# Kernel optimization log

Hardware: AMD Instinct MI355X
Metric: run time of the kernel (lower is better)

Reference implementation:

```python
import jax, jax.numpy as jnp
import numpy as np

DIM, N_HEADS, HEAD_DIM, BASE = 1024, 16, 64, 10000.0
B, S = 2, 2048


def setup_inputs() -> dict:
    key = jax.random.key(0)
    ks = jax.random.split(key, 8)
    theta = (BASE ** (-jnp.arange(0, HEAD_DIM, 2, dtype=jnp.float32) / HEAD_DIM))  # [head_dim//2]
    s = 0.02
    return {
        "x": jax.random.normal(ks[0], (B, S, DIM), jnp.float32),
        "positions": jnp.arange(S, dtype=jnp.int32),
        "theta": theta,
        "Wq": jax.random.normal(ks[1], (DIM, N_HEADS * HEAD_DIM), jnp.float32) * s,
        "bq": jnp.zeros((N_HEADS * HEAD_DIM,), jnp.float32),
        "Wk": jax.random.normal(ks[2], (DIM, N_HEADS * HEAD_DIM), jnp.float32) * s,
        "bk": jnp.zeros((N_HEADS * HEAD_DIM,), jnp.float32),
        "Wv": jax.random.normal(ks[3], (DIM, N_HEADS * HEAD_DIM), jnp.float32) * s,
        "bv": jnp.zeros((N_HEADS * HEAD_DIM,), jnp.float32),
        "Wo": jax.random.normal(ks[4], (N_HEADS * HEAD_DIM, DIM), jnp.float32) * s,
        "bo": jnp.zeros((DIM,), jnp.float32),
    }


def _rope(x, theta):
    # x: [B, H, S, head_dim]; theta: [head_dim//2]
    seq_len = x.shape[2]
    ang = jnp.arange(seq_len, dtype=x.dtype)[:, None] * theta  # [S, head_dim//2]
    cos = jnp.cos(ang)[None, None]  # [1,1,S,head_dim//2]
    sin = jnp.sin(ang)[None, None]
    x1, x2 = x[..., 0::2], x[..., 1::2]
    # matches torch.cat([-x2*sin + x1*cos, x1*sin + x2*cos], dim=-1)
    return jnp.concatenate([x1 * cos - x2 * sin, x1 * sin + x2 * cos], axis=-1)


def reference(x, positions, theta, Wq, bq, Wk, bk, Wv, bv, Wo, bo):
    batch, seq_len, _ = x.shape
    H, hd = N_HEADS, HEAD_DIM

    def split_heads(t):
        return t.reshape(batch, seq_len, H, hd).transpose(0, 2, 1, 3)  # [B,H,S,hd]

    q = split_heads(x @ Wq + bq)
    k = split_heads(x @ Wk + bk)
    v = split_heads(x @ Wv + bv)
    q = _rope(q, theta)
    k = _rope(k, theta)

    scale = 1.0 / jnp.sqrt(jnp.asarray(hd, x.dtype))
    scores = jnp.einsum("bhqd,bhkd->bhqk", q, k) * scale  # [B,H,S,S]
    causal = jnp.tril(jnp.ones((seq_len, seq_len), dtype=bool))
    scores = jnp.where(causal, scores, jnp.asarray(-jnp.inf, x.dtype))
    attn = jax.nn.softmax(scores, axis=-1)  # dropout is identity at eval
    out = jnp.einsum("bhqk,bhkd->bhqd", attn, v)  # [B,H,S,hd]
    out = out.transpose(0, 2, 1, 3).reshape(batch, seq_len, H * hd)
    return out @ Wo + bo
```

## Files before the change

kernel.cpp:

```cpp
#include <hip/hip_runtime.h>
#include <math.h>

#define B_   2
#define S_   2048
#define DIM_ 1024
#define H_   16
#define HD_  64
#define BS_  (B_ * S_)
#define BHSD ((size_t)B_ * H_ * S_ * HD_)
#define CEXP 0.1803368801111244f

typedef unsigned short u16;
typedef unsigned int   u32;
typedef short s16x8 __attribute__((ext_vector_type(8)));
typedef float f32x4 __attribute__((ext_vector_type(4)));

#define MFMA16(a, b, c) __builtin_amdgcn_mfma_f32_16x16x32_bf16((a), (b), (c), 0, 0, 0)

__device__ __forceinline__ u16 f2bf(float f) {
    u32 u = __float_as_uint(f);
    u += 0x7fffu + ((u >> 16) & 1u);
    return (u16)(u >> 16);
}
__device__ __forceinline__ u32 cvt_pk_bf16(float a, float b) {
    u32 r;
    asm("v_cvt_pk_bf16_f32 %0, %1, %2" : "=v"(r) : "v"(a), "v"(b));
    return r;
}
__device__ __forceinline__ void gl16(void* lds, const void* g) {
    __builtin_amdgcn_global_load_lds(
        (__attribute__((address_space(1))) void*)(g),
        (__attribute__((address_space(3))) void*)(lds), 16, 0, 0);
}

__global__ __launch_bounds__(256) void prep(
    const float* __restrict__ x, u16* __restrict__ xb,
    const float* __restrict__ W0, const float* __restrict__ W1,
    const float* __restrict__ W2, const float* __restrict__ W3,
    u16* __restrict__ T0, u16* __restrict__ T1,
    u16* __restrict__ T2, u16* __restrict__ T3,
    const float* __restrict__ bq, const float* __restrict__ bk,
    const float* __restrict__ bv, float* __restrict__ bias3,
    const float* __restrict__ theta, float2* __restrict__ cs)
{
    __shared__ float tile[32][33];
    const int bid = blockIdx.x, tid = threadIdx.x;

    if (bid < 2048) {
        const int i = bid * 256 + tid;
        const float4 a = *(const float4*)(x + (size_t)i * 8);
        const float4 b = *(const float4*)(x + (size_t)i * 8 + 4);
        s16x8 o;
        o[0] = (short)f2bf(a.x); o[1] = (short)f2bf(a.y);
        o[2] = (short)f2bf(a.z); o[3] = (short)f2bf(a.w);
        o[4] = (short)f2bf(b.x); o[5] = (short)f2bf(b.y);
        o[6] = (short)f2bf(b.z); o[7] = (short)f2bf(b.w);
        *(s16x8*)(xb + (size_t)i * 8) = o;
    } else if (bid < 6144) {
        const int idx = bid - 2048;
        const int z = idx >> 10;
        const float* W; u16* T;
        switch (z) {
            case 0: W = W0; T = T0; break;
            case 1: W = W1; T = T1; break;
            case 2: W = W2; T = T2; break;
            default: W = W3; T = T3; break;
        }
        const int n0 = ((idx >> 5) & 31) * 32, k0 = (idx & 31) * 32;
        const int c = tid & 31, rr = tid >> 5;
#pragma unroll
        for (int i = 0; i < 4; ++i) {
            const int k = rr + i * 8;
            tile[k][c] = W[(size_t)(k0 + k) * DIM_ + n0 + c];
        }
        __syncthreads();
#pragma unroll
        for (int i = 0; i < 4; ++i) {
            const int col = n0 + rr + i * 8;
            int pcol = col;
            if (z < 2) {
                const int dd = col & 63;
                const int pd = (dd & 1) ? 32 + (dd >> 1) : (dd >> 1);
                pcol = (col & ~63) | pd;
            }
            T[(size_t)pcol * DIM_ + k0 + c] = f2bf(tile[c][rr + i * 8]);
        }
    } else if (bid < 6400) {
        const int idx = bid - 6144;
        const int s = idx * 8 + (tid >> 5), j = tid & 31;
        float sn, cn;
        sincosf((float)s * theta[j], &sn, &cn);
        cs[(s << 5) + j] = make_float2(cn, sn);
    } else {
        const int i = (bid - 6400) * 256 + tid;
        const int which = i >> 10, local = i & 1023;
        const float v = (which == 0) ? bq[local]
                      : (which == 1) ? bk[local] : bv[local];
        int dst = i;
        if (which < 2) {
            const int dd = local & 63;
            const int pd = (dd & 1) ? 32 + (dd >> 1) : (dd >> 1);
            dst = which * 1024 + (local & ~63) + pd;
        }
        bias3[dst] = v;
    }
}

template<int BN, int HMIN, int EPI>
__global__ __launch_bounds__(256, 3) void gemm_mfma(
    const u16* __restrict__ A, const u16* __restrict__ Bt,
    const float* __restrict__ bias, void* __restrict__ Yv,
    const float2* __restrict__ cs)
{
    __shared__ u16 As[128 * 64];
    __shared__ u16 Bs[BN * 64];

    const int tid = threadIdx.x, lane = tid & 63, wid = tid >> 6;
    const int l15 = lane & 15, lg = lane >> 4;
    const int row0 = blockIdx.x * 128, col0 = blockIdx.y * BN;
    const int wr = (wid >> 1) * 64;
    const int wc = (wid & 1) * (BN / 2);
    constexpr int NM = 4, NN = BN / 32, BCH = BN / 32;

    const int l8 = lane >> 3, l7 = lane & 7;
    const int colE = ((l7 ^ l8) << 3);

    const u16* aptr[4]; u16* aldp[4];
#pragma unroll
    for (int i = 0; i < 4; ++i) {
        const int ci = wid * 4 + i;
        const int rr = row0 + ci * 8 + l8;
        size_t a0;
        if (HMIN)
            a0 = (((size_t)(rr >> 11) * H_) * S_ + (rr & (S_ - 1))) * HD_ + colE;
        else
            a0 = (size_t)rr * DIM_ + colE;
        aptr[i] = A + a0;
        aldp[i] = As + ci * 512;
    }
    const u16* bptr[BCH]; u16* bldp[BCH];
#pragma unroll
    for (int i = 0; i < BCH; ++i) {
        const int ci = wid * BCH + i;
        const int rr = col0 + ci * 8 + l8;
        bptr[i] = Bt + (size_t)rr * DIM_ + colE;
        bldp[i] = Bs + ci * 512;
    }
    const size_t astep = HMIN ? (size_t)S_ * HD_ : 64;

    f32x4 acc[NM][NN];
#pragma unroll
    for (int m = 0; m < NM; ++m)
#pragma unroll
        for (int n = 0; n < NN; ++n) acc[m][n] = (f32x4){0.f, 0.f, 0.f, 0.f};

    for (int k0 = 0; k0 < DIM_; k0 += 64) {
        __syncthreads();
#pragma unroll
        for (int i = 0; i < 4; ++i) gl16(aldp[i], aptr[i]);
#pragma unroll
        for (int i = 0; i < BCH; ++i) gl16(bldp[i], bptr[i]);
#pragma unroll
        for (int i = 0; i < 4; ++i) aptr[i] += astep;
#pragma unroll
        for (int i = 0; i < BCH; ++i) bptr[i] += 64;
        __syncthreads();

        s16x8 af[NM][2], bfr[NN][2];
#pragma unroll
        for (int m = 0; m < NM; ++m) {
            const int row = wr + m * 16 + l15;
#pragma unroll
            for (int kf = 0; kf < 2; ++kf)
                af[m][kf] = *(const s16x8*)&As[row * 64 +
                    (((kf * 64 + lg * 16) ^ ((l15 & 7) << 4)) >> 1)];
        }
#pragma unroll
        for (int n = 0; n < NN; ++n) {
            const int row = wc + n * 16 + l15;
#pragma unroll
            for (int kf = 0; kf < 2; ++kf)
                bfr[n][kf] = *(const s16x8*)&Bs[row * 64 +
                    (((kf * 64 + lg * 16) ^ ((l15 & 7) << 4)) >> 1)];
        }
        __builtin_amdgcn_s_setprio(1);
#pragma unroll
        for (int m = 0; m < NM; ++m)
#pragma unroll
            for (int n = 0; n < NN; ++n) {
                acc[m][n] = MFMA16(af[m][0], bfr[n][0], acc[m][n]);
                acc[m][n] = MFMA16(af[m][1], bfr[n][1], acc[m][n]);
            }
        __builtin_amdgcn_s_setprio(0);
    }

    if (EPI == 0) {
        u16* Y = (u16*)Yv;
        const int whichq = (col0 + wc) >> 10;
        if (whichq < 2) {
            const float sclw = (whichq == 0) ? CEXP : 1.0f;
#pragma unroll
            for (int n = 0; n < 2; ++n) {
                const int cc0 = col0 + wc + n * 16 + l15;
                const int j = n * 16 + l15;
                const float bv0 = bias[cc0];
                const float bv1 = bias[cc0 + 32];
                const int hh = (cc0 >> 6) & (H_ - 1);
#pragma unroll
                for (int m = 0; m < NM; ++m)
#pragma unroll
                    for (int r = 0; r < 4; ++r) {
                        const int rr = row0 + wr + m * 16 + lg * 4 + r;
                        const int b = rr >> 11, s = rr & (S_ - 1);
                        const float2 csv = cs[(s << 5) + j];
                        const float v0 = acc[m][n][r] + bv0;
                        const float v1 = acc[m][n + 2][r] + bv1;
                        const size_t base = (size_t)whichq * BHSD
                            + (((size_t)b * H_ + hh) * S_ + s) * HD_;
                        Y[base + j]      = f2bf((v0 * csv.x - v1 * csv.y) * sclw);
                        Y[base + j + 32] = f2bf((v0 * csv.y + v1 * csv.x) * sclw);
                    }
            }
        } else {
#pragma unroll
            for (int n = 0; n < NN; ++n) {
                const int cc = col0 + wc + n * 16 + l15;
                const float bv = bias[cc];
                const int hh = (cc >> 6) & (H_ - 1), d = cc & 63;
#pragma unroll
                for (int m = 0; m < NM; ++m)
#pragma unroll
                    for (int r = 0; r < 4; ++r) {
                        const int rr = row0 + wr + m * 16 + lg * 4 + r;
                        const int b = rr >> 11, s = rr & (S_ - 1);
                        const int sp = (s & ~60) | ((s & 12) << 1)
                                     | ((s & 16) << 1) | ((s & 32) >> 3);
                        Y[2 * BHSD + ((size_t)(b * H_ + hh) * HD_ + d) * S_ + sp] =
                            f2bf(acc[m][n][r] + bv);
                    }
            }
        }
    } else {
#pragma unroll
        for (int n = 0; n < NN; ++n) {
            const int cc = col0 + wc + n * 16 + l15;
            const float bv = bias[cc];
#pragma unroll
            for (int m = 0; m < NM; ++m)
#pragma unroll
                for (int r = 0; r < 4; ++r) {
                    const int rr = row0 + wr + m * 16 + lg * 4 + r;
                    ((float*)Yv)[(size_t)rr * DIM_ + cc] = acc[m][n][r] + bv;
                }
        }
    }
}

__global__ __launch_bounds__(256, 4) void attn_q(
    u16* __restrict__ Q, const u16* __restrict__ K, const u16* __restrict__ VT)
{
    const int bh = blockIdx.x;
    const int y  = blockIdx.y;
    const int a = y >> 3, r_ = y & 7;
    const int qt = (a == 0) ? (31 - r_) : (a == 1) ? (16 + r_)
                 : (a == 2) ? (15 - r_) : r_;
    const int nsteps = qt + 1;

    u16* Qg = Q + (size_t)bh * S_ * HD_;
    const u16* Kg = K + (size_t)bh * S_ * HD_;
    const u16* Vg = VT + (size_t)bh * HD_ * S_;

    __shared__ u16 Ks[2][64 * 64];
    __shared__ u16 Vs[2][64 * 64];

    const int tid = threadIdx.x;
    const int w = tid >> 6, lane = tid & 63;
    const int q0 = qt * 64 + w * 16;
    const int l15 = lane & 15, lg = lane >> 4;

    const int crow = lane >> 3, cslt = lane & 7;

    auto stage = [&](int bufi, int j0) {
#pragma unroll
        for (int i = 0; i < 2; ++i) {
            const int c = w * 2 + i;
            const int row = c * 8 + crow;
            const int soff = ((cslt ^ (row & 7)) << 3);
            gl16(&Ks[bufi][c * 512], Kg + (size_t)(j0 + row) * HD_ + soff);
            gl16(&Vs[bufi][c * 512], Vg + (size_t)row * S_ + j0 + soff);
        }
    };

    s16x8 qf[2];
    {
        const u16* qrow = Qg + (size_t)(q0 + l15) * HD_ + lg * 8;
        qf[0] = *(const s16x8*)(qrow);
        qf[1] = *(const s16x8*)(qrow + 32);
    }

    s16x8 onesv;
#pragma unroll
    for (int i = 0; i < 8; ++i) onesv[i] = (short)0x3F80;

    f32x4 o[4], ol;
#pragma unroll
    for (int n = 0; n < 4; ++n) o[n] = (f32x4){0.f, 0.f, 0.f, 0.f};
    ol = (f32x4){0.f, 0.f, 0.f, 0.f};

    stage(0, 0);
    __syncthreads();

    int buf = 0;
    for (int t = 0; t < nsteps; ++t) {
        if (t + 1 < nsteps) stage(buf ^ 1, (t + 1) * 64);

        const u16* Kb = Ks[buf];
        const u16* Vb = Vs[buf];

        f32x4 sc[4];
        __builtin_amdgcn_s_setprio(1);
#pragma unroll
        for (int sub = 0; sub < 4; ++sub) {
            const int kr = sub * 16 + l15;
            const s16x8 kf0 = *(const s16x8*)&Kb[kr * 64 + ((lg ^ (kr & 7)) << 3)];
            const s16x8 kf1 = *(const s16x8*)&Kb[kr * 64 + (((lg + 4) ^ (kr & 7)) << 3)];
            f32x4 z = (f32x4){0.f, 0.f, 0.f, 0.f};
            z = MFMA16(kf0, qf[0], z);
            sc[sub] = MFMA16(kf1, qf[1], z);
        }
        __builtin_amdgcn_s_setprio(0);

        if (t == qt) {
#pragma unroll
            for (int sub = 0; sub < 4; ++sub) {
                if (sub == w) {
#pragma unroll
                    for (int r = 0; r < 4; ++r)
                        if (lg * 4 + r > l15) sc[sub][r] = -1e30f;
                } else if (sub > w) {
#pragma unroll
                    for (int r = 0; r < 4; ++r) sc[sub][r] = -1e30f;
                }
            }
        }

        float p[4][4];
#pragma unroll
        for (int sub = 0; sub < 4; ++sub)
#pragma unroll
            for (int r = 0; r < 4; ++r)
                p[sub][r] = __builtin_amdgcn_exp2f(sc[sub][r]);

        union { s16x8 v; u32 w4[4]; } af[2];
#pragma unroll
        for (int step = 0; step < 2; ++step)
#pragma unroll
            for (int jj = 0; jj < 4; ++jj) {
                const int sub = (jj >> 1) * 2 + step;
                const int r0  = (jj & 1) * 2;
                af[step].w4[jj] = cvt_pk_bf16(p[sub][r0], p[sub][r0 + 1]);
            }
        __builtin_amdgcn_s_setprio(1);
#pragma unroll
        for (int n = 0; n < 4; ++n) {
            const int d = n * 16 + l15;
            const s16x8 vf0 = *(const s16x8*)&Vb[d * 64 + ((lg ^ (d & 7)) << 3)];
            const s16x8 vf1 = *(const s16x8*)&Vb[d * 64 + (((lg + 4) ^ (d & 7)) << 3)];
            o[n] = MFMA16(af[0].v, vf0, o[n]);
            o[n] = MFMA16(af[1].v, vf1, o[n]);
        }
        ol = MFMA16(af[0].v, onesv, ol);
        ol = MFMA16(af[1].v, onesv, ol);
        __builtin_amdgcn_s_setprio(0);

        __syncthreads();
        buf ^= 1;
    }

    f32x4 il;
#pragma unroll
    for (int r = 0; r < 4; ++r) il[r] = 1.f / ol[r];
    u16* orow = Qg + (size_t)(q0 + lg * 4) * HD_ + l15;
#pragma unroll
    for (int r = 0; r < 4; ++r)
#pragma unroll
        for (int n = 0; n < 4; ++n)
            orow[r * HD_ + n * 16] = f2bf(o[n][r] * il[r]);
}

extern "C" void kernel_launch(void* const* d_in, const int* in_sizes, int n_in,
                              void* d_out, int out_size, void* d_ws, size_t ws_size,
                              hipStream_t stream)
{
    (void)in_sizes; (void)n_in; (void)out_size; (void)ws_size;
    const float* x     = (const float*)d_in[0];
    const float* theta = (const float*)d_in[2];
    const float* Wq    = (const float*)d_in[3];
    const float* bq    = (const float*)d_in[4];
    const float* Wk    = (const float*)d_in[5];
    const float* bk    = (const float*)d_in[6];
    const float* Wv    = (const float*)d_in[7];
    const float* bv    = (const float*)d_in[8];
    const float* Wo    = (const float*)d_in[9];
    const float* bo    = (const float*)d_in[10];
    float* out = (float*)d_out;

    u16* xb  = (u16*)d_ws;
    u16* wtq = xb + (size_t)BS_ * DIM_;
    u16* wtk = wtq + (size_t)DIM_ * DIM_;
    u16* wtv = wtk + (size_t)DIM_ * DIM_;
    u16* wto = wtv + (size_t)DIM_ * DIM_;
    u16* qws = wto + (size_t)DIM_ * DIM_;
    u16* kws = qws + BHSD;
    u16* vtw = kws + BHSD;
    float* bias3 = (float*)(vtw + BHSD);
    float2* cs = (float2*)(bias3 + 4096);

    prep<<<dim3(6412), dim3(256), 0, stream>>>(
        x, xb, Wq, Wk, Wv, Wo, wtq, wtk, wtv, wto, bq, bk, bv, bias3, theta, cs);

    gemm_mfma<128, 0, 0><<<dim3(32, 24), dim3(256), 0, stream>>>(
        xb, wtq, bias3, qws, cs);

    attn_q<<<dim3(32, 32), dim3(256), 0, stream>>>(qws, kws, vtw);

    gemm_mfma<64, 1, 1><<<dim3(32, 16), dim3(256), 0, stream>>>(
        qws, wto, bo, out, cs);
}
```

Measured before the change: 91.54 us.

## Rewrite attention kernel with 32x32 MFMA and split-K wave layout

Replaces the 16x16x32 MFMA attention inner loop with 32x32x16 MFMAs, splitting four waves into 2 query halves by 2 key halves. Each wave skips fully masked diagonal sub-tiles, computes row sums with shuffles instead of a ones-vector MFMA, and the two key-half partial outputs are combined through LDS at the end. The V-transpose permutation in the projection epilogue is changed to match the new operand layout. This adds a final LDS reduction and a bf16 rounding of the partial output, and increases register pressure from the larger accumulators.

New measurement: 94.17 us. 1.03x slower.

```diff
diff --git a/kernel.cpp b/kernel.cpp
--- a/kernel.cpp
+++ b/kernel.cpp
@@ -14,13 +14,18 @@
 typedef unsigned int   u32;
 typedef short s16x8 __attribute__((ext_vector_type(8)));
 typedef float f32x4 __attribute__((ext_vector_type(4)));
+typedef float f32x16 __attribute__((ext_vector_type(16)));
 
 #define MFMA16(a, b, c) __builtin_amdgcn_mfma_f32_16x16x32_bf16((a), (b), (c), 0, 0, 0)
+#define MFMA32(a, b, c) __builtin_amdgcn_mfma_f32_32x32x16_bf16((a), (b), (c), 0, 0, 0)
 
 __device__ __forceinline__ u16 f2bf(float f) {
     u32 u = __float_as_uint(f);
     u += 0x7fffu + ((u >> 16) & 1u);
     return (u16)(u >> 16);
+}
+__device__ __forceinline__ float bf2f(u16 h) {
+    return __uint_as_float(((u32)h) << 16);
 }
 __device__ __forceinline__ u32 cvt_pk_bf16(float a, float b) {
     u32 r;
@@ -233,8 +238,7 @@
                     for (int r = 0; r < 4; ++r) {
                         const int rr = row0 + wr + m * 16 + lg * 4 + r;
                         const int b = rr >> 11, s = rr & (S_ - 1);
-                        const int sp = (s & ~60) | ((s & 12) << 1)
-                                     | ((s & 16) << 1) | ((s & 32) >> 3);
+                        const int sp = (s & ~12) | ((s & 4) << 1) | ((s & 8) >> 1);
                         Y[2 * BHSD + ((size_t)(b * H_ + hh) * HD_ + d) * S_ + sp] =
                             f2bf(acc[m][n][r] + bv);
                     }
@@ -256,7 +260,7 @@
     }
 }
 
-__global__ __launch_bounds__(256, 4) void attn_q(
+__global__ __launch_bounds__(256, 4) void attn32(
     u16* __restrict__ Q, const u16* __restrict__ K, const u16* __restrict__ VT)
 {
     const int bh = blockIdx.x;
@@ -275,37 +279,36 @@
 
     const int tid = threadIdx.x;
     const int w = tid >> 6, lane = tid & 63;
-    const int q0 = qt * 64 + w * 16;
-    const int l15 = lane & 15, lg = lane >> 4;
-
-    const int crow = lane >> 3, cslt = lane & 7;
-
+    const int wq = w & 1, wk = w >> 1;
+    const int l31 = lane & 31, h = lane >> 5;
+    const int swz = l31 & 7;
+    const int q0 = qt * 64 + wq * 32;
+    const int krow = wk * 32 + l31;
+
+    const int crw = lane >> 3, cslt = lane & 7;
     auto stage = [&](int bufi, int j0) {
 #pragma unroll
         for (int i = 0; i < 2; ++i) {
             const int c = w * 2 + i;
-            const int row = c * 8 + crow;
+            const int row = c * 8 + crw;
             const int soff = ((cslt ^ (row & 7)) << 3);
             gl16(&Ks[bufi][c * 512], Kg + (size_t)(j0 + row) * HD_ + soff);
             gl16(&Vs[bufi][c * 512], Vg + (size_t)row * S_ + j0 + soff);
         }
     };
 
-    s16x8 qf[2];
+    s16x8 qf[4];
     {
-        const u16* qrow = Qg + (size_t)(q0 + l15) * HD_ + lg * 8;
-        qf[0] = *(const s16x8*)(qrow);
-        qf[1] = *(const s16x8*)(qrow + 32);
-    }
-
-    s16x8 onesv;
-#pragma unroll
-    for (int i = 0; i < 8; ++i) onesv[i] = (short)0x3F80;
-
-    f32x4 o[4], ol;
-#pragma unroll
-    for (int n = 0; n < 4; ++n) o[n] = (f32x4){0.f, 0.f, 0.f, 0.f};
-    ol = (f32x4){0.f, 0.f, 0.f, 0.f};
+        const u16* qrow = Qg + (size_t)(q0 + l31) * HD_ + h * 8;
+#pragma unroll
+        for (int ks = 0; ks < 4; ++ks)
+            qf[ks] = *(const s16x8*)(qrow + ks * 16);
+    }
+
+    f32x16 o0, o1;
+#pragma unroll
+    for (int r = 0; r < 16; ++r) { o0[r] = 0.f; o1[r] = 0.f; }
+    float lI = 0.f;
 
     stage(0, 0);
     __syncthreads();
@@ -314,78 +317,86 @@
     for (int t = 0; t < nsteps; ++t) {
         if (t + 1 < nsteps) stage(buf ^ 1, (t + 1) * 64);
 
-        const u16* Kb = Ks[buf];
-        const u16* Vb = Vs[buf];
-
-        f32x4 sc[4];
-        __builtin_amdgcn_s_setprio(1);
-#pragma unroll
-        for (int sub = 0; sub < 4; ++sub) {
-            const int kr = sub * 16 + l15;
-            const s16x8 kf0 = *(const s16x8*)&Kb[kr * 64 + ((lg ^ (kr & 7)) << 3)];
-            const s16x8 kf1 = *(const s16x8*)&Kb[kr * 64 + (((lg + 4) ^ (kr & 7)) << 3)];
-            f32x4 z = (f32x4){0.f, 0.f, 0.f, 0.f};
-            z = MFMA16(kf0, qf[0], z);
-            sc[sub] = MFMA16(kf1, qf[1], z);
-        }
-        __builtin_amdgcn_s_setprio(0);
-
-        if (t == qt) {
-#pragma unroll
-            for (int sub = 0; sub < 4; ++sub) {
-                if (sub == w) {
-#pragma unroll
-                    for (int r = 0; r < 4; ++r)
-                        if (lg * 4 + r > l15) sc[sub][r] = -1e30f;
-                } else if (sub > w) {
-#pragma unroll
-                    for (int r = 0; r < 4; ++r) sc[sub][r] = -1e30f;
+        if (t < qt || wk <= wq) {
+            const u16* Kb = Ks[buf];
+            const u16* Vb = Vs[buf];
+
+            f32x16 sc;
+#pragma unroll
+            for (int r = 0; r < 16; ++r) sc[r] = 0.f;
+            __builtin_amdgcn_s_setprio(1);
+#pragma unroll
+            for (int ks = 0; ks < 4; ++ks) {
+                const s16x8 kf = *(const s16x8*)&Kb[krow * 64 +
+                    ((((ks << 1) | h) ^ swz) << 3)];
+                sc = MFMA32(kf, qf[ks], sc);
+            }
+            __builtin_amdgcn_s_setprio(0);
+
+            if (t == qt && wk == wq) {
+#pragma unroll
+                for (int r = 0; r < 16; ++r) {
+                    const int cr = (r & 3) + 8 * (r >> 2) + 4 * h;
+                    if (cr > l31) sc[r] = -1e30f;
                 }
             }
-        }
-
-        float p[4][4];
-#pragma unroll
-        for (int sub = 0; sub < 4; ++sub)
-#pragma unroll
-            for (int r = 0; r < 4; ++r)
-                p[sub][r] = __builtin_amdgcn_exp2f(sc[sub][r]);
-
-        union { s16x8 v; u32 w4[4]; } af[2];
-#pragma unroll
-        for (int step = 0; step < 2; ++step)
-#pragma unroll
-            for (int jj = 0; jj < 4; ++jj) {
-                const int sub = (jj >> 1) * 2 + step;
-                const int r0  = (jj & 1) * 2;
-                af[step].w4[jj] = cvt_pk_bf16(p[sub][r0], p[sub][r0 + 1]);
-            }
-        __builtin_amdgcn_s_setprio(1);
-#pragma unroll
-        for (int n = 0; n < 4; ++n) {
-            const int d = n * 16 + l15;
-            const s16x8 vf0 = *(const s16x8*)&Vb[d * 64 + ((lg ^ (d & 7)) << 3)];
-            const s16x8 vf1 = *(const s16x8*)&Vb[d * 64 + (((lg + 4) ^ (d & 7)) << 3)];
-            o[n] = MFMA16(af[0].v, vf0, o[n]);
-            o[n] = MFMA16(af[1].v, vf1, o[n]);
-        }
-        ol = MFMA16(af[0].v, onesv, ol);
-        ol = MFMA16(af[1].v, onesv, ol);
-        __builtin_amdgcn_s_setprio(0);
+
+            float p[16];
+            float ps = 0.f;
+#pragma unroll
+            for (int r = 0; r < 16; ++r) {
+                p[r] = __builtin_amdgcn_exp2f(sc[r]);
+                ps += p[r];
+            }
+            ps += __shfl_xor(ps, 32);
+            lI += ps;
+
+            __builtin_amdgcn_s_setprio(1);
+#pragma unroll
+            for (int m = 0; m < 2; ++m) {
+                union { s16x8 v; u32 w4[4]; } pa;
+#pragma unroll
+                for (int q2 = 0; q2 < 4; ++q2)
+                    pa.w4[q2] = cvt_pk_bf16(p[m * 8 + q2 * 2],
+                                            p[m * 8 + q2 * 2 + 1]);
+                const int sl = ((wk * 4 + m * 2 + h) ^ swz) << 3;
+                const s16x8 v0 = *(const s16x8*)&Vb[l31 * 64 + sl];
+                const s16x8 v1 = *(const s16x8*)&Vb[(32 + l31) * 64 + sl];
+                o0 = MFMA32(pa.v, v0, o0);
+                o1 = MFMA32(pa.v, v1, o1);
+            }
+            __builtin_amdgcn_s_setprio(0);
+        }
 
         __syncthreads();
         buf ^= 1;
     }
 
-    f32x4 il;
-#pragma unroll
-    for (int r = 0; r < 4; ++r) il[r] = 1.f / ol[r];
-    u16* orow = Qg + (size_t)(q0 + lg * 4) * HD_ + l15;
-#pragma unroll
-    for (int r = 0; r < 4; ++r)
-#pragma unroll
-        for (int n = 0; n < 4; ++n)
-            orow[r * HD_ + n * 16] = f2bf(o[n][r] * il[r]);
+    u16* Om = &Ks[0][0];
+    float* Lm = (float*)&Vs[0][0];
+    if (wk == 1) {
+#pragma unroll
+        for (int r = 0; r < 16; ++r) {
+            const int cr = (r & 3) + 8 * (r >> 2) + 4 * h;
+            Om[(wq * 32 + cr) * 64 + l31]      = f2bf(o0[r]);
+            Om[(wq * 32 + cr) * 64 + 32 + l31] = f2bf(o1[r]);
+        }
+        if (lane < 32) Lm[wq * 32 + l31] = lI;
+    }
+    __syncthreads();
+    if (wk == 0) {
+        const float il = 1.f / (lI + Lm[wq * 32 + l31]);
+#pragma unroll
+        for (int r = 0; r < 16; ++r) {
+            const int cr = (r & 3) + 8 * (r >> 2) + 4 * h;
+            const float ilr = __shfl(il, cr);
+            u16* orow = Qg + (size_t)(q0 + cr) * HD_;
+            const float a0 = o0[r] + bf2f(Om[(wq * 32 + cr) * 64 + l31]);
+            const float a1 = o1[r] + bf2f(Om[(wq * 32 + cr) * 64 + 32 + l31]);
+            orow[l31]      = f2bf(a0 * ilr);
+            orow[32 + l31] = f2bf(a1 * ilr);
+        }
+    }
 }
 
 extern "C" void kernel_launch(void* const* d_in, const int* in_sizes, int n_in,
@@ -422,7 +433,7 @@
     gemm_mfma<128, 0, 0><<<dim3(32, 24), dim3(256), 0, stream>>>(
         xb, wtq, bias3, qws, cs);
 
-    attn_q<<<dim3(32, 32), dim3(256), 0, stream>>>(qws, kws, vtw);
+    attn32<<<dim3(32, 32), dim3(256), 0, stream>>>(qws, kws, vtw);
 
     gemm_mfma<64, 1, 1><<<dim3(32, 16), dim3(256), 0, stream>>>(
         qws, wto, bo, out, cs);
```
